# Kernel tuning notes

Hardware: AMD Instinct MI355X
Metric: run time of the kernel (lower is better)

The kernel has to match this reference:

```python
import jax, jax.numpy as jnp
import numpy as np

SEQ, BATCH, INP = 20, 16384, 2
HID, EMB = 256, 64
TARGET_LEN = 30


def setup_inputs() -> dict:
    key = jax.random.key(0)
    ks = jax.random.split(key, 12)
    s = 0.1
    return {
        "x_input": jax.random.normal(ks[0], (SEQ, BATCH, INP), dtype=jnp.float32),
        # encoder embedding Linear(input_size -> emb_dim)
        "W_emb": jax.random.normal(ks[1], (EMB, INP), dtype=jnp.float32) * s,
        "b_emb": jax.random.normal(ks[2], (EMB,), dtype=jnp.float32) * s,
        # encoder LSTM (input EMB -> hidden HID), PyTorch gate order i,f,g,o; bias = b_ih + b_hh
        "W_ih_enc": jax.random.normal(ks[3], (4 * HID, EMB), dtype=jnp.float32) * s,
        "W_hh_enc": jax.random.normal(ks[4], (4 * HID, HID), dtype=jnp.float32) * s,
        "b_enc": jax.random.normal(ks[5], (4 * HID,), dtype=jnp.float32) * s,
        # decoder LSTM (input INP -> hidden HID)
        "W_ih_dec": jax.random.normal(ks[6], (4 * HID, INP), dtype=jnp.float32) * s,
        "W_hh_dec": jax.random.normal(ks[7], (4 * HID, HID), dtype=jnp.float32) * s,
        "b_dec": jax.random.normal(ks[8], (4 * HID,), dtype=jnp.float32) * s,
        # decoder output Linear(hidden -> input_size)
        "W_out": jax.random.normal(ks[9], (INP, HID), dtype=jnp.float32) * s,
        "b_out": jax.random.normal(ks[10], (INP,), dtype=jnp.float32) * s,
        "target_len": TARGET_LEN,
    }


def _lstm_cell(x, h, c, W_ih, W_hh, b):
    # x: [B, in], h/c: [B, H]; PyTorch gate order: input, forget, cell(g), output
    gates = x @ W_ih.T + h @ W_hh.T + b  # [B, 4H]
    i, f, g, o = jnp.split(gates, 4, axis=-1)
    c_new = jax.nn.sigmoid(f) * c + jax.nn.sigmoid(i) * jnp.tanh(g)
    h_new = jax.nn.sigmoid(o) * jnp.tanh(c_new)
    return h_new, c_new


def reference(x_input, W_emb, b_emb, W_ih_enc, W_hh_enc, b_enc,
              W_ih_dec, W_hh_dec, b_dec, W_out, b_out, target_len):
    B = x_input.shape[1]
    # --- encoder ---
    x_emb = x_input @ W_emb.T + b_emb  # [S, B, EMB]
    h0 = jnp.zeros((B, HID), dtype=x_input.dtype)
    c0 = jnp.zeros((B, HID), dtype=x_input.dtype)

    def enc_step(carry, xt):
        h, c = carry
        h, c = _lstm_cell(xt, h, c, W_ih_enc, W_hh_enc, b_enc)
        return (h, c), None

    (h_enc, c_enc), _ = jax.lax.scan(enc_step, (h0, c0), x_emb)

    dec_in0 = x_input[-1]  # [B, INP]

    def dec_step(carry, _):
        di, h, c = carry
        h, c = _lstm_cell(di, h, c, W_ih_dec, W_hh_dec, b_dec)
        out = h @ W_out.T + b_out  # [B, INP]
        return (out, h, c), out

    _, outputs = jax.lax.scan(dec_step, (dec_in0, h_enc, c_enc), None,
                              length=int(target_len))
    return outputs  # [target_len, B, INP]
```

## Files before the change

kernel.cpp:

```cpp
#include <hip/hip_runtime.h>


#define SEQ  20
#define TLEN 30
#define LOG2E  1.442695041f
#define LOG2E2 2.885390082f

typedef _Float16 half8   __attribute__((ext_vector_type(8)));
typedef _Float16 half4   __attribute__((ext_vector_type(4)));
typedef float    floatx4 __attribute__((ext_vector_type(4)));

__device__ _Float16 g_w_enc[1024 * 288];
__device__ _Float16 g_w_dec0[1024 * 288];
__device__ _Float16 g_w_deff[1024 * 288];
__device__ _Float16 g_wout[512];

__global__ void prep_kernel(const float* __restrict__ W_emb,
                            const float* __restrict__ b_emb,
                            const float* __restrict__ W_ih_enc,
                            const float* __restrict__ W_hh_enc,
                            const float* __restrict__ b_enc,
                            const float* __restrict__ W_ih_dec,
                            const float* __restrict__ W_hh_dec,
                            const float* __restrict__ b_dec,
                            const float* __restrict__ W_out,
                            const float* __restrict__ b_out) {
    int gid = blockIdx.x * blockDim.x + threadIdx.x;
    int stride = gridDim.x * blockDim.x;
    for (int s = gid; s < 1024 * 288; s += stride) {
        int n = s / 288, k = s - n * 288;
        int g = n >> 8, c = (n >> 4) & 15, l16 = n & 15;
        int w = c >> 1, cc = c & 1;
        int i = cc * 4 + g;
        int kt = k >> 5, q = (k >> 3) & 3, j = k & 7;
        int dst = ((w * 9 + kt) * 8 + i) * 512 + q * 128 + l16 * 8 + j;
        float sc = (g == 2) ? LOG2E2 : LOG2E;
        float fe = 0.f, fd = 0.f, ff = 0.f;
        if (k < 256) {
            fe = W_hh_enc[n * 256 + k];
            fd = W_hh_dec[n * 256 + k];
            ff = fd + W_ih_dec[2 * n] * W_out[k]
                    + W_ih_dec[2 * n + 1] * W_out[256 + k];
        } else {
            int kp = k - 256;
            if (kp < 2) {
                fd = W_ih_dec[2 * n + kp];
                const float* wr = &W_ih_enc[n * 64];
                for (int e = 0; e < 64; e++) fe = fmaf(wr[e], W_emb[2 * e + kp], fe);
            } else if (kp == 2) {
                fd = b_dec[n];
                ff = b_dec[n] + W_ih_dec[2 * n] * b_out[0]
                              + W_ih_dec[2 * n + 1] * b_out[1];
                fe = b_enc[n];
                const float* wr = &W_ih_enc[n * 64];
                for (int e = 0; e < 64; e++) fe = fmaf(wr[e], b_emb[e], fe);
            }
        }
        g_w_enc[dst]  = (_Float16)(fe * sc);
        g_w_dec0[dst] = (_Float16)(fd * sc);
        g_w_deff[dst] = (_Float16)(ff * sc);
    }
    if (gid < 512) g_wout[gid] = (_Float16)W_out[gid];
}

__global__ __launch_bounds__(512, 2) void lstm_fused(
        const float* __restrict__ x_input,
        const float* __restrict__ b_out,
        float* __restrict__ out)
{
    __shared__ __align__(16) _Float16 h_pack[2][18432];
    __shared__ __align__(16) float    partial_lds[2][8 * 132];

    const int tid = threadIdx.x;
    const int w   = tid >> 6;
    const int L   = tid & 63;
    const int l16 = L & 15;
    const int q   = L >> 4;
    const long row0 = (long)blockIdx.x * 64;

    {
        int* hz = (int*)&h_pack[0][0];
        for (int idx = tid; idx < 18432; idx += 512) hz[idx] = 0;
    }
    __syncthreads();
    if (tid < 128) {
        int buf = tid >> 6, b = tid & 63;
        h_pack[buf][((b >> 4) * 9 + 8) * 512 + (b & 15) * 8 + 2] = (_Float16)1.f;
    }
    if (tid < 128) {
        int b = tid >> 1, jj = tid & 1;
        h_pack[0][((b >> 4) * 9 + 8) * 512 + (b & 15) * 8 + jj] =
            (_Float16)x_input[(row0 + b) * 2 + jj];
    }

    const float bo = b_out[tid & 1];
    const int aoff = q * 128 + l16 * 8;
    const _Float16* __restrict__ wenc_w  = &g_w_enc[w * 36864];
    const _Float16* __restrict__ wdec0_w = &g_w_dec0[w * 36864];
    const _Float16* __restrict__ wdeff_w = &g_w_deff[w * 36864];

    _Float16 wo[2][2][4];
#pragma unroll
    for (int jj = 0; jj < 2; jj++)
#pragma unroll
        for (int cc = 0; cc < 2; cc++)
#pragma unroll
            for (int r = 0; r < 4; r++)
                wo[jj][cc][r] = g_wout[jj * 256 + 32 * w + 16 * cc + 4 * q + r];

    floatx4 acc[8][4];
    float   c_st[4][2][4];
#pragma unroll
    for (int nt = 0; nt < 4; nt++)
#pragma unroll
        for (int cc = 0; cc < 2; cc++)
#pragma unroll
            for (int r = 0; r < 4; r++) c_st[nt][cc][r] = 0.f;

    __syncthreads();

    int cur = 0;
#pragma unroll 1
    for (int t = 0; t < SEQ + TLEN; t++) {
        const _Float16* __restrict__ Wb =
            (t < SEQ) ? wenc_w : (t == SEQ) ? wdec0_w : wdeff_w;
        const _Float16* __restrict__ hp = h_pack[cur];
        _Float16* __restrict__ hn = h_pack[cur ^ 1];

#pragma unroll
        for (int kt = 0; kt < 9; kt++) {
            half8 B[4];
#pragma unroll
            for (int nt = 0; nt < 4; nt++)
                B[nt] = *(const half8*)&hp[(nt * 9 + kt) * 512 + aoff];
#pragma unroll
            for (int i = 0; i < 8; i++) {
                half8 Aw = *(const half8*)&Wb[(kt * 8 + i) * 512 + aoff];
                if (kt == 0) {
#pragma unroll
                    for (int nt = 0; nt < 4; nt++)
                        acc[i][nt] = __builtin_amdgcn_mfma_f32_16x16x32_f16(
                            Aw, B[nt], (floatx4)(0.f), 0, 0, 0);
                } else {
#pragma unroll
                    for (int nt = 0; nt < 4; nt++)
                        acc[i][nt] = __builtin_amdgcn_mfma_f32_16x16x32_f16(
                            Aw, B[nt], acc[i][nt], 0, 0, 0);
                }
            }
        }

        float xval = 0.f;
        if (t < SEQ && tid < 128) {
            int srct = (t + 1 < SEQ) ? t + 1 : SEQ - 1;
            xval = x_input[(long)srct * 32768 + (row0 + (tid >> 1)) * 2 + (tid & 1)];
        }

        const bool dec = (t >= SEQ);
        float po[4][2];
#pragma unroll
        for (int nt = 0; nt < 4; nt++) { po[nt][0] = 0.f; po[nt][1] = 0.f; }

#pragma unroll
        for (int nt = 0; nt < 4; nt++)
#pragma unroll
            for (int cc = 0; cc < 2; cc++) {
                half4 hv4;
                float hvf[4];
#pragma unroll
                for (int r = 0; r < 4; r++) {
                    float ai = acc[cc * 4 + 0][nt][r];
                    float af = acc[cc * 4 + 1][nt][r];
                    float ag = acc[cc * 4 + 2][nt][r];
                    float ao = acc[cc * 4 + 3][nt][r];
                    float eI = __builtin_amdgcn_exp2f(-ai);
                    float eG = __builtin_amdgcn_exp2f(-ag);
                    float eF = __builtin_amdgcn_exp2f(-af);
                    float eO = __builtin_amdgcn_exp2f(-ao);
                    float ig = (1.f - eG) *
                        __builtin_amdgcn_rcpf((1.f + eI) * (1.f + eG));
                    float fs = __builtin_amdgcn_rcpf(1.f + eF);
                    float cn = fmaf(fs, c_st[nt][cc][r], ig);
                    c_st[nt][cc][r] = cn;
                    float cnc = fminf(fmaxf(cn, -12.f), 12.f);
                    float eC = __builtin_amdgcn_exp2f(-LOG2E2 * cnc);
                    float hv = (1.f - eC) *
                        __builtin_amdgcn_rcpf((1.f + eO) * (1.f + eC));
                    hvf[r] = hv;
                    hv4[r] = (_Float16)hv;
                }
                *(half4*)&hn[(nt * 9 + w) * 512 + (2 * cc + (q >> 1)) * 128 +
                             l16 * 8 + 4 * (q & 1)] = hv4;
                if (dec) {
#pragma unroll
                    for (int r = 0; r < 4; r++) {
                        po[nt][0] = fmaf(hvf[r], (float)wo[0][cc][r], po[nt][0]);
                        po[nt][1] = fmaf(hvf[r], (float)wo[1][cc][r], po[nt][1]);
                    }
                }
            }

        if (dec) {
#pragma unroll
            for (int nt = 0; nt < 4; nt++)
#pragma unroll
                for (int jj = 0; jj < 2; jj++) {
                    float s = po[nt][jj];
                    s += __shfl_xor(s, 16);
                    s += __shfl_xor(s, 32);
                    po[nt][jj] = s;
                }
            if (q == 0) {
                float* pl = &partial_lds[t & 1][w * 132];
#pragma unroll
                for (int nt = 0; nt < 4; nt++) {
                    pl[nt * 16 + l16]      = po[nt][0];
                    pl[66 + nt * 16 + l16] = po[nt][1];
                }
            }
        }

        if (t < SEQ && tid < 128) {
            int b = tid >> 1, jj = tid & 1;
            hn[((b >> 4) * 9 + 8) * 512 + (b & 15) * 8 + jj] = (_Float16)xval;
        }

        __syncthreads();

        if (dec && tid < 128) {
            int m = tid >> 1, jj = tid & 1;
            const float* pl = &partial_lds[t & 1][jj * 66 + m];
            float s = bo;
#pragma unroll
            for (int w8 = 0; w8 < 8; w8++) s += pl[w8 * 132];
            out[(long)(t - SEQ) * 32768 + (row0 + m) * 2 + jj] = s;
        }

        cur ^= 1;
    }
}

extern "C" void kernel_launch(void* const* d_in, const int* in_sizes, int n_in,
                              void* d_out, int out_size, void* d_ws, size_t ws_size,
                              hipStream_t stream) {
    (void)in_sizes; (void)n_in; (void)d_ws; (void)ws_size; (void)out_size;
    const float* x      = (const float*)d_in[0];
    const float* W_emb  = (const float*)d_in[1];
    const float* b_emb  = (const float*)d_in[2];
    const float* W_ih_e = (const float*)d_in[3];
    const float* W_hh_e = (const float*)d_in[4];
    const float* b_enc  = (const float*)d_in[5];
    const float* W_ih_d = (const float*)d_in[6];
    const float* W_hh_d = (const float*)d_in[7];
    const float* b_dec  = (const float*)d_in[8];
    const float* W_out  = (const float*)d_in[9];
    const float* b_out  = (const float*)d_in[10];
    float* outp = (float*)d_out;

    prep_kernel<<<512, 256, 0, stream>>>(W_emb, b_emb, W_ih_e, W_hh_e, b_enc,
                                         W_ih_d, W_hh_d, b_dec, W_out, b_out);
    lstm_fused<<<256, 512, 0, stream>>>(x, b_out, outp);
}
```

Measured before the change: 599.9 us.

## Stage first weight k-tile in LDS, fold decoder bias into MFMA accumulator init

Caches the first 8-row k-tile of each wave's weights in shared memory, reloading it at the encoder/decoder transitions. In steady decoder steps it folds the precomputed bias into the initial MFMA accumulator and skips the ninth k-tile, whose only work is the bias/input column. It also fuses the forget and input sigmoid reciprocals into a single reciprocal for the cell update and hoists the x_input load. The goal is less global weight traffic and fewer MFMAs and transcendental ops per step, at the cost of 64KB+ extra LDS, which may reduce occupancy below two blocks per CU.

```diff
diff --git a/kernel.cpp b/kernel.cpp
--- a/kernel.cpp
+++ b/kernel.cpp
@@ -14,6 +14,7 @@
 __device__ _Float16 g_w_dec0[1024 * 288];
 __device__ _Float16 g_w_deff[1024 * 288];
 __device__ _Float16 g_wout[512];
+__device__ float    g_bias_dec[1024];
 
 __global__ void prep_kernel(const float* __restrict__ W_emb,
                             const float* __restrict__ b_emb,
@@ -54,6 +55,7 @@
                 fe = b_enc[n];
                 const float* wr = &W_ih_enc[n * 64];
                 for (int e = 0; e < 64; e++) fe = fmaf(wr[e], b_emb[e], fe);
+                g_bias_dec[(w * 8 + i) * 16 + l16] = ff * sc;
             }
         }
         g_w_enc[dst]  = (_Float16)(fe * sc);
@@ -70,6 +72,8 @@
 {
     __shared__ __align__(16) _Float16 h_pack[2][18432];
     __shared__ __align__(16) float    partial_lds[2][8 * 132];
+    __shared__ __align__(16) _Float16 w_lds[32768];
+    __shared__ __align__(16) float    bias_lds[1024];
 
     const int tid = threadIdx.x;
     const int w   = tid >> 6;
@@ -82,6 +86,14 @@
         int* hz = (int*)&h_pack[0][0];
         for (int idx = tid; idx < 18432; idx += 512) hz[idx] = 0;
     }
+    {
+        const half8* __restrict__ gsrc = (const half8*)&g_w_enc[w * 36864];
+        half8* ldst = (half8*)&w_lds[w * 4096];
+#pragma unroll
+        for (int r8 = 0; r8 < 8; r8++) ldst[r8 * 64 + L] = gsrc[r8 * 64 + L];
+    }
+    bias_lds[tid]       = g_bias_dec[tid];
+    bias_lds[tid + 512] = g_bias_dec[tid + 512];
     __syncthreads();
     if (tid < 128) {
         int buf = tid >> 6, b = tid & 63;
@@ -124,36 +136,49 @@
     for (int t = 0; t < SEQ + TLEN; t++) {
         const _Float16* __restrict__ Wb =
             (t < SEQ) ? wenc_w : (t == SEQ) ? wdec0_w : wdeff_w;
+        const bool skip8 = (t > SEQ);
         const _Float16* __restrict__ hp = h_pack[cur];
         _Float16* __restrict__ hn = h_pack[cur ^ 1];
-
-#pragma unroll
-        for (int kt = 0; kt < 9; kt++) {
-            half8 B[4];
-#pragma unroll
-            for (int nt = 0; nt < 4; nt++)
-                B[nt] = *(const half8*)&hp[(nt * 9 + kt) * 512 + aoff];
-#pragma unroll
-            for (int i = 0; i < 8; i++) {
-                half8 Aw = *(const half8*)&Wb[(kt * 8 + i) * 512 + aoff];
-                if (kt == 0) {
-#pragma unroll
-                    for (int nt = 0; nt < 4; nt++)
-                        acc[i][nt] = __builtin_amdgcn_mfma_f32_16x16x32_f16(
-                            Aw, B[nt], (floatx4)(0.f), 0, 0, 0);
-                } else {
-#pragma unroll
-                    for (int nt = 0; nt < 4; nt++)
-                        acc[i][nt] = __builtin_amdgcn_mfma_f32_16x16x32_f16(
-                            Aw, B[nt], acc[i][nt], 0, 0, 0);
-                }
-            }
-        }
 
         float xval = 0.f;
         if (t < SEQ && tid < 128) {
             int srct = (t + 1 < SEQ) ? t + 1 : SEQ - 1;
             xval = x_input[(long)srct * 32768 + (row0 + (tid >> 1)) * 2 + (tid & 1)];
+        }
+
+#pragma unroll
+        for (int kt = 0; kt < 9; kt++) {
+            if (kt < 8 || !skip8) {
+                half8 B[4];
+#pragma unroll
+                for (int nt = 0; nt < 4; nt++)
+                    B[nt] = *(const half8*)&hp[(nt * 9 + kt) * 512 + aoff];
+#pragma unroll
+                for (int i = 0; i < 8; i++) {
+                    if (kt == 0) {
+                        half8 Aw = *(const half8*)&w_lds[w * 4096 + i * 512 + aoff];
+                        if (skip8) {
+                            floatx4 bfr = *(const floatx4*)
+                                &bias_lds[(w * 8 + i) * 16 + q * 4];
+#pragma unroll
+                            for (int nt = 0; nt < 4; nt++)
+                                acc[i][nt] = __builtin_amdgcn_mfma_f32_16x16x32_f16(
+                                    Aw, B[nt], bfr, 0, 0, 0);
+                        } else {
+#pragma unroll
+                            for (int nt = 0; nt < 4; nt++)
+                                acc[i][nt] = __builtin_amdgcn_mfma_f32_16x16x32_f16(
+                                    Aw, B[nt], (floatx4)(0.f), 0, 0, 0);
+                        }
+                    } else {
+                        half8 Aw = *(const half8*)&Wb[(kt * 8 + i) * 512 + aoff];
+#pragma unroll
+                        for (int nt = 0; nt < 4; nt++)
+                            acc[i][nt] = __builtin_amdgcn_mfma_f32_16x16x32_f16(
+                                Aw, B[nt], acc[i][nt], 0, 0, 0);
+                    }
+                }
+            }
         }
 
         const bool dec = (t >= SEQ);
@@ -174,13 +199,15 @@
                     float ag = acc[cc * 4 + 2][nt][r];
                     float ao = acc[cc * 4 + 3][nt][r];
                     float eI = __builtin_amdgcn_exp2f(-ai);
+                    float eF = __builtin_amdgcn_exp2f(-af);
                     float eG = __builtin_amdgcn_exp2f(-ag);
-                    float eF = __builtin_amdgcn_exp2f(-af);
                     float eO = __builtin_amdgcn_exp2f(-ao);
-                    float ig = (1.f - eG) *
-                        __builtin_amdgcn_rcpf((1.f + eI) * (1.f + eG));
-                    float fs = __builtin_amdgcn_rcpf(1.f + eF);
-                    float cn = fmaf(fs, c_st[nt][cc][r], ig);
+                    float a1 = 1.f + eI;
+                    float a2 = 1.f + eG;
+                    float a3 = 1.f + eF;
+                    float t1 = a1 * a2;
+                    float num = fmaf(c_st[nt][cc][r], t1, (1.f - eG) * a3);
+                    float cn  = num * __builtin_amdgcn_rcpf(t1 * a3);
                     c_st[nt][cc][r] = cn;
                     float cnc = fminf(fmaxf(cn, -12.f), 12.f);
                     float eC = __builtin_amdgcn_exp2f(-LOG2E2 * cnc);
@@ -223,6 +250,15 @@
         if (t < SEQ && tid < 128) {
             int b = tid >> 1, jj = tid & 1;
             hn[((b >> 4) * 9 + 8) * 512 + (b & 15) * 8 + jj] = (_Float16)xval;
+        }
+
+        if (t == SEQ - 1 || t == SEQ) {
+            const _Float16* __restrict__ wsrc =
+                (t == SEQ - 1) ? &g_w_dec0[w * 36864] : &g_w_deff[w * 36864];
+            const half8* __restrict__ gsrc = (const half8*)wsrc;
+            half8* ldst = (half8*)&w_lds[w * 4096];
+#pragma unroll 2
+            for (int r8 = 0; r8 < 8; r8++) ldst[r8 * 64 + L] = gsrc[r8 * 64 + L];
         }
 
         __syncthreads();
```

Result: slower. 666.1 us (+11.0%).
